# Kernel optimization log

Hardware: AMD Instinct MI355X
Metric: run time of the kernel (lower is better)

The kernel has to match this reference:

```python
import jax, jax.numpy as jnp
import numpy as np

DEPTH = 8
DIM = 512
D_INNER = 2 * DIM          # mamba expand=2
D_STATE = 16
D_CONV = 4
DT_RANK = DIM // 16        # 32
B, H, W = 2, 16, 16
EPS = 1e-5


def setup_inputs() -> dict:
    key = jax.random.key(0)
    ks = jax.random.split(key, 8)
    s = 0.02
    f32 = jnp.float32
    x = jax.random.normal(ks[0], (B, DIM, H, W), f32)
    in_proj_w = (jax.random.normal(ks[1], (DEPTH, 2 * D_INNER, DIM), f32) * s)
    conv_w = (jax.random.normal(ks[2], (DEPTH, D_INNER, D_CONV), f32) * 0.1)
    conv_b = jnp.zeros((DEPTH, D_INNER), f32)
    x_proj_w = (jax.random.normal(ks[3], (DEPTH, DT_RANK + 2 * D_STATE, D_INNER), f32) * s)
    dt_proj_w = (jax.random.normal(ks[4], (DEPTH, D_INNER, DT_RANK), f32) * s)
    dt_proj_b = (jax.random.normal(ks[5], (DEPTH, D_INNER), f32) * 0.1)
    # S4D-real init: A = -exp(A_log), A_log = log(1..d_state)
    A_log = jnp.log(jnp.broadcast_to(
        jnp.arange(1, D_STATE + 1, dtype=f32), (DEPTH, D_INNER, D_STATE)))
    D = jnp.ones((DEPTH, D_INNER), f32)
    out_proj_w = (jax.random.normal(ks[6], (DEPTH, DIM, D_INNER), f32) * s)
    norm_w = jnp.ones((DEPTH, DIM), f32)
    final_norm_w = jnp.ones((DIM,), f32)
    return {"x": x, "in_proj_w": in_proj_w, "conv_w": conv_w, "conv_b": conv_b,
            "x_proj_w": x_proj_w, "dt_proj_w": dt_proj_w, "dt_proj_b": dt_proj_b,
            "A_log": A_log, "D": D, "out_proj_w": out_proj_w,
            "norm_w": norm_w, "final_norm_w": final_norm_w}


def _rmsnorm(x, w):
    # rms_norm_ref: no mean subtraction, weight only (bias is None)
    return x * jax.lax.rsqrt(jnp.mean(x * x, axis=-1, keepdims=True) + EPS) * w


def _mixer(h, Wi, cw, cb, Wx, Wdt, bdt, A_log, Dv, Wo):
    # h: [B, L, DIM]
    xz = jnp.einsum('bld,ed->ble', h, Wi)            # [B,L,2*Di]
    xc, z = jnp.split(xz, 2, axis=-1)
    # causal depthwise conv1d (pad left d_conv-1), then SiLU
    xt = xc.transpose(0, 2, 1)                        # [B,Di,L]
    xt = jax.lax.conv_general_dilated(
        xt, cw[:, None, :], (1,), [(D_CONV - 1, 0)],
        feature_group_count=D_INNER)
    xc = jax.nn.silu((xt + cb[None, :, None]).transpose(0, 2, 1))  # [B,L,Di]
    dbl = jnp.einsum('bld,kd->blk', xc, Wx)           # [B,L,dt_rank+2N]
    dtr = dbl[..., :DT_RANK]
    Bm = dbl[..., DT_RANK:DT_RANK + D_STATE]          # [B,L,N]
    Cm = dbl[..., DT_RANK + D_STATE:]                 # [B,L,N]
    dt = jax.nn.softplus(jnp.einsum('blr,dr->bld', dtr, Wdt) + bdt)  # [B,L,Di]
    A = -jnp.exp(A_log)                               # [Di,N]
    dA = jnp.exp(dt[..., None] * A)                   # [B,L,Di,N]
    dBx = (dt * xc)[..., None] * Bm[:, :, None, :]    # [B,L,Di,N]

    def step(s, inp):
        a, bx, c = inp
        s = a * s + bx                                # [B,Di,N]
        return s, jnp.einsum('bdn,bn->bd', s, c)

    s0 = jnp.zeros((xc.shape[0], D_INNER, D_STATE), xc.dtype)
    _, ys = jax.lax.scan(step, s0, (dA.transpose(1, 0, 2, 3),
                                    dBx.transpose(1, 0, 2, 3),
                                    Cm.transpose(1, 0, 2)))
    y = ys.transpose(1, 0, 2) + Dv * xc               # [B,L,Di]
    y = y * jax.nn.silu(z)
    return jnp.einsum('bld,od->blo', y, Wo)           # [B,L,DIM]


def reference(x, in_proj_w, conv_w, conv_b, x_proj_w, dt_proj_w, dt_proj_b,
              A_log, D, out_proj_w, norm_w, final_norm_w):
    Bz, C, Hh, Ww = x.shape
    h = x.reshape(Bz, C, Hh * Ww).transpose(0, 2, 1)  # [B,L,C]
    residual = None
    for i in range(DEPTH):
        # fused add + RMSNorm (prenorm): residual <- h + residual; hn = norm(residual)
        residual = h if residual is None else h + residual
        hn = _rmsnorm(residual, norm_w[i])
        h = _mixer(hn, in_proj_w[i], conv_w[i], conv_b[i], x_proj_w[i],
                   dt_proj_w[i], dt_proj_b[i], A_log[i], D[i], out_proj_w[i])
    # Original module: with return_index=[depth-1], the returned tensor is the
    # post-loop `residual`; the final mixer output and final norm are dead code.
    out = residual.reshape(Bz, Hh, Ww, C)
    return out.transpose(0, 3, 1, 2)
```

## Files before the change

### kernel.cpp

```cpp
#include <hip/hip_runtime.h>
#include <hip/hip_bf16.h>

typedef __bf16 bf16x8 __attribute__((ext_vector_type(8)));
typedef float  f32x4  __attribute__((ext_vector_type(4)));
typedef unsigned short ushort8v __attribute__((ext_vector_type(8)));

#define DIM    512
#define DINNER 1024
#define SEQL   256
#define NLAYER 7
#define LPAD   260
#define NCH    8
#define CLEN   32

#define N4WI (NLAYER * 2048 * 512 / 4)
#define N4WX (NLAYER * 64 * 1024 / 4)
#define N4WO (NLAYER * 512 * 1024 / 4)
#define N4ALL (N4WI + N4WX + N4WO)
#define NCASTB (N4ALL / 256)

__global__ __launch_bounds__(256) void k_castin(const float* __restrict__ Wi,
                                                const float* __restrict__ Wx,
                                                const float* __restrict__ Wo,
                                                const float* __restrict__ x,
                                                __hip_bfloat16* __restrict__ wib,
                                                __hip_bfloat16* __restrict__ wxb,
                                                __hip_bfloat16* __restrict__ wob,
                                                float* __restrict__ res) {
  if (blockIdx.x >= NCASTB) {
    int idx = (blockIdx.x - NCASTB) * 256 + threadIdx.x;
    int d = idx & (DIM - 1), l = (idx >> 9) & (SEQL - 1), b = idx >> 17;
    res[idx] = x[((size_t)((b << 9) + d) << 8) + l];
    return;
  }
  int i = blockIdx.x * 256 + threadIdx.x;
  const float* src; __hip_bfloat16* dst; int j;
  if (i < N4WI)             { src = Wi; dst = wib; j = i; }
  else if (i < N4WI + N4WX) { src = Wx; dst = wxb; j = i - N4WI; }
  else                      { src = Wo; dst = wob; j = i - N4WI - N4WX; }
  float4 v = reinterpret_cast<const float4*>(src)[j];
  struct alignas(8) B4 { __hip_bfloat16 a, b, c, d; };
  B4 o{ (__hip_bfloat16)v.x, (__hip_bfloat16)v.y, (__hip_bfloat16)v.z, (__hip_bfloat16)v.w };
  reinterpret_cast<B4*>(dst)[j] = o;
}

__global__ __launch_bounds__(1024) void k_front(const float* __restrict__ res,
                                                const float* __restrict__ nwL,
                                                const __hip_bfloat16* __restrict__ wiL,
                                                const float4* __restrict__ cwL,
                                                const float* __restrict__ cbL,
                                                __hip_bfloat16* __restrict__ xcb,
                                                float* __restrict__ zT) {
  __shared__ __align__(16) char smem[75264];
  __hip_bfloat16 (*s_hn)[520] = (__hip_bfloat16(*)[520])smem;
  float (*s_xz)[132] = (float(*)[132])(smem + 49920);
  const int tid = threadIdx.x, bid = blockIdx.x;
  const int wid = tid >> 6, lane = tid & 63;
  const int r = lane & 15, g = lane >> 4;
  const int ttile = bid >> 4, sl = bid & 15;
  const int t0 = ttile * 32, m0 = t0 - 3;
#pragma unroll
  for (int k = 0; k < 3; ++k) {
    int rw = wid * 3 + k;
    int grc = min(max(m0 + rw, 0), 511);
    const float* rr = res + ((size_t)grc << 9);
    float v[8]; float ssum = 0.f;
#pragma unroll
    for (int j2 = 0; j2 < 8; ++j2) { v[j2] = rr[lane + (j2 << 6)]; ssum = fmaf(v[j2], v[j2], ssum); }
#pragma unroll
    for (int m = 1; m < 64; m <<= 1) ssum += __shfl_xor(ssum, m);
    float inv = rsqrtf(ssum * (1.0f / 512.0f) + 1e-5f);
#pragma unroll
    for (int j2 = 0; j2 < 8; ++j2)
      s_hn[rw][lane + (j2 << 6)] = (__hip_bfloat16)(v[j2] * inv * nwL[lane + (j2 << 6)]);
  }
  __syncthreads();
  for (int j = wid; j < 24; j += 16) {
    int mf = j >> 3, cf = j & 7;
    int gcol = (cf < 4) ? (sl * 64 + cf * 16 + r) : (1024 + sl * 64 + (cf - 4) * 16 + r);
    const bf16x8* pb = reinterpret_cast<const bf16x8*>(wiL + (size_t)gcol * 512) + g;
    f32x4 acc = {0.f, 0.f, 0.f, 0.f};
#pragma unroll
    for (int kc = 0; kc < 16; ++kc) {
      bf16x8 a = *reinterpret_cast<const bf16x8*>(&s_hn[mf * 16 + r][kc * 32 + g * 8]);
      acc = __builtin_amdgcn_mfma_f32_16x16x32_bf16(a, pb[kc * 4], acc, 0, 0, 0);
    }
    int cc = (cf < 4) ? (cf * 16 + r) : (64 + (cf - 4) * 16 + r);
#pragma unroll
    for (int jj = 0; jj < 4; ++jj) s_xz[mf * 16 + g * 4 + jj][cc] = acc[jj];
  }
  __syncthreads();
  const int t0s = t0 & 255;
#pragma unroll
  for (int k = 0; k < 2; ++k) {
    int e = tid + (k << 10);
    int lloc = e >> 6, c = e & 63;
    int gd = sl * 64 + c;
    int lseq = t0s + lloc;
    float4 wv = cwL[gd];
    float accv = cbL[gd];
    accv = fmaf(s_xz[lloc + 3][c], wv.w, accv);
    if (lseq >= 1) accv = fmaf(s_xz[lloc + 2][c], wv.z, accv);
    if (lseq >= 2) accv = fmaf(s_xz[lloc + 1][c], wv.y, accv);
    if (lseq >= 3) accv = fmaf(s_xz[lloc + 0][c], wv.x, accv);
    float sv = accv / (1.f + __expf(-accv));
    xcb[(size_t)(t0 + lloc) * 1024 + gd] = (__hip_bfloat16)sv;
  }
  __syncthreads();
#pragma unroll
  for (int k = 0; k < 2; ++k) {
    int e = tid + (k << 10);
    int lloc = e & 31, c = e >> 5;
    int gd = sl * 64 + c;
    zT[(size_t)gd * 512 + t0 + lloc] = s_xz[lloc + 3][64 + c];
  }
}

__global__ __launch_bounds__(1024) void k_xdt(const __hip_bfloat16* __restrict__ xcb,
                                              const __hip_bfloat16* __restrict__ wxL,
                                              float* __restrict__ dblBC,
                                              __hip_bfloat16* __restrict__ dtrb) {
  __shared__ __align__(16) float s_red[4 * 1088];
  const int tid = threadIdx.x, bid = blockIdx.x;
  const int wid = tid >> 6, lane = tid & 63;
  const int r = lane & 15, g = lane >> 4;
  const int t0 = bid * 16;
  {
    int nf = wid >> 2, ks = wid & 3;
    const bf16x8* pa = reinterpret_cast<const bf16x8*>(xcb + (size_t)(t0 + r) * 1024) + ks * 32 + g;
    const bf16x8* pb = reinterpret_cast<const bf16x8*>(wxL + (size_t)(nf * 16 + r) * 1024) + ks * 32 + g;
    f32x4 acc = {0.f, 0.f, 0.f, 0.f};
#pragma unroll
    for (int kc = 0; kc < 8; ++kc)
      acc = __builtin_amdgcn_mfma_f32_16x16x32_bf16(pa[kc * 4], pb[kc * 4], acc, 0, 0, 0);
#pragma unroll
    for (int jj = 0; jj < 4; ++jj)
      s_red[ks * 1088 + (g * 4 + jj) * 68 + nf * 16 + r] = acc[jj];
  }
  __syncthreads();
  {
    int row = tid >> 6, col = tid & 63;
    float dsum = s_red[row * 68 + col] + s_red[1088 + row * 68 + col]
               + s_red[2176 + row * 68 + col] + s_red[3264 + row * 68 + col];
    if (col >= 32) dblBC[((size_t)(t0 + row) << 5) + (col - 32)] = dsum;
    else           dtrb [((size_t)(t0 + row) << 5) + col] = (__hip_bfloat16)dsum;
  }
}

__global__ __launch_bounds__(1024) void k_scan(const float* __restrict__ dblBC,
                                               const __hip_bfloat16* __restrict__ dtrb,
                                               const float* __restrict__ WdtL,
                                               const float* __restrict__ bdtL,
                                               const __hip_bfloat16* __restrict__ xcb,
                                               const float* __restrict__ zT,
                                               const float* __restrict__ alog,
                                               const float* __restrict__ dv,
                                               __hip_bfloat16* __restrict__ y) {
  __shared__ __align__(16) char smem[127744];
  float (*s_dt)[LPAD] = (float(*)[LPAD])(smem);
  float (*s_xc)[LPAD] = (float(*)[LPAD])(smem + 8320);
  float (*s_B)[LPAD]  = (float(*)[LPAD])(smem + 16640);
  float (*s_C)[LPAD]  = (float(*)[LPAD])(smem + 33280);
  float (*s_cp)[68]   = (float(*)[68]) (smem + 49920);
  float (*s_pe)[128]  = (float(*)[128])(smem + 119552);
  float (*s_se)[128]  = (float(*)[128])(smem + 123648);
  const int tid = threadIdx.x, bid = blockIdx.x;
  const int cg = tid >> 7;
  const int tt = tid & 127;
  const int n = tt & 15, dl = tt >> 4;
  const int b = bid >> 7;
  const int d0 = (bid & 127) << 3;
  const int d = d0 + dl;
  const int bL = b * SEQL;

#pragma unroll
  for (int k = 0; k < 2; ++k) {
    int fidx = tid + (k << 10);
    int l = fidx >> 3, q = fidx & 7;
    float4 v = *reinterpret_cast<const float4*>(dblBC + ((size_t)(bL + l) << 5) + (q << 2));
    float* dst = (q < 4) ? &s_B[(q & 3) << 2][l] : &s_C[(q & 3) << 2][l];
    dst[0] = v.x; dst[LPAD] = v.y; dst[2 * LPAD] = v.z; dst[3 * LPAD] = v.w;
  }
  if (tid < 256) {
    bf16x8 u = *reinterpret_cast<const bf16x8*>(xcb + (size_t)(bL + tid) * 1024 + d0);
#pragma unroll
    for (int e = 0; e < 8; ++e) s_xc[e][tid] = (float)u[e];
  }
  {
    int tk = tid >> 2;
    int cp = (tid & 3) << 1;
    const ushort8v* drp = reinterpret_cast<const ushort8v*>(
        reinterpret_cast<const unsigned short*>(dtrb) + ((size_t)(bL + tk) << 5));
    float xv[32];
#pragma unroll
    for (int q = 0; q < 4; ++q) {
      ushort8v u = drp[q];
#pragma unroll
      for (int e = 0; e < 8; ++e)
        xv[q * 8 + e] = __uint_as_float(((unsigned int)u[e]) << 16);
    }
#pragma unroll
    for (int kk = 0; kk < 2; ++kk) {
      int ch = cp + kk;
      const float4* wr = reinterpret_cast<const float4*>(WdtL + ((size_t)(d0 + ch) << 5));
      float acc = bdtL[d0 + ch];
#pragma unroll
      for (int q = 0; q < 8; ++q) {
        float4 w = wr[q];
        acc = fmaf(xv[q * 4 + 0], w.x, acc);
        acc = fmaf(xv[q * 4 + 1], w.y, acc);
        acc = fmaf(xv[q * 4 + 2], w.z, acc);
        acc = fmaf(xv[q * 4 + 3], w.w, acc);
      }
      s_dt[ch][tk] = (acc > 20.f) ? acc : log1pf(__expf(acc));
    }
  }
  __syncthreads();

  const float An = -__expf(alog[(size_t)d * 16 + n]);
  const int lb = cg << 5;

  float s = 0.f, P = 1.f;
#pragma unroll 2
  for (int l4 = 0; l4 < CLEN; l4 += 4) {
    const int l = lb + l4;
    float4 dt4 = *reinterpret_cast<const float4*>(&s_dt[dl][l]);
    float4 xc4 = *reinterpret_cast<const float4*>(&s_xc[dl][l]);
    float4 B4  = *reinterpret_cast<const float4*>(&s_B[n][l]);
    float dA;
    dA = __expf(dt4.x * An); P *= dA; s = fmaf(dA, s, dt4.x * xc4.x * B4.x);
    dA = __expf(dt4.y * An); P *= dA; s = fmaf(dA, s, dt4.y * xc4.y * B4.y);
    dA = __expf(dt4.z * An); P *= dA; s = fmaf(dA, s, dt4.z * xc4.z * B4.z);
    dA = __expf(dt4.w * An); P *= dA; s = fmaf(dA, s, dt4.w * xc4.w * B4.w);
  }
  s_pe[cg][tt] = P;
  s_se[cg][tt] = s;
  __syncthreads();

  float ss = 0.f;
  for (int c = 0; c < cg; ++c) ss = fmaf(s_pe[c][tt], ss, s_se[c][tt]);

  float s2 = ss;
#pragma unroll 2
  for (int l4 = 0; l4 < CLEN; l4 += 4) {
    const int l = lb + l4;
    float4 dt4 = *reinterpret_cast<const float4*>(&s_dt[dl][l]);
    float4 xc4 = *reinterpret_cast<const float4*>(&s_xc[dl][l]);
    float4 B4  = *reinterpret_cast<const float4*>(&s_B[n][l]);
    float4 C4  = *reinterpret_cast<const float4*>(&s_C[n][l]);
    float dA, c;
    dA = __expf(dt4.x * An); s2 = fmaf(dA, s2, dt4.x * xc4.x * B4.x); c = s2 * C4.x;
    c += __shfl_xor(c, 1); if (!(n & 1)) s_cp[l + 0][(dl << 3) | (n >> 1)] = c;
    dA = __expf(dt4.y * An); s2 = fmaf(dA, s2, dt4.y * xc4.y * B4.y); c = s2 * C4.y;
    c += __shfl_xor(c, 1); if (!(n & 1)) s_cp[l + 1][(dl << 3) | (n >> 1)] = c;
    dA = __expf(dt4.z * An); s2 = fmaf(dA, s2, dt4.z * xc4.z * B4.z); c = s2 * C4.z;
    c += __shfl_xor(c, 1); if (!(n & 1)) s_cp[l + 2][(dl << 3) | (n >> 1)] = c;
    dA = __expf(dt4.w * An); s2 = fmaf(dA, s2, dt4.w * xc4.w * B4.w); c = s2 * C4.w;
    c += __shfl_xor(c, 1); if (!(n & 1)) s_cp[l + 3][(dl << 3) | (n >> 1)] = c;
  }
  __syncthreads();

#pragma unroll
  for (int k = 0; k < 2; ++k) {
    int idx = tid + (k << 10);
    int l = idx >> 3, dd = idx & 7;
    const float* cr = &s_cp[l][dd << 3];
    float4 a0 = *reinterpret_cast<const float4*>(cr);
    float4 a1 = *reinterpret_cast<const float4*>(cr + 4);
    float sum = ((a0.x + a0.y) + (a0.z + a0.w)) + ((a1.x + a1.y) + (a1.z + a1.w));
    float xcv = s_xc[dd][l];
    float zv = zT[(size_t)(d0 + dd) * 512 + bL + l];
    float yv = (sum + dv[d0 + dd] * xcv) * (zv / (1.f + __expf(-zv)));
    y[((size_t)(bL + l) << 10) + d0 + dd] = (__hip_bfloat16)yv;
  }
}

template <bool FINAL>
__global__ __launch_bounds__(1024) void k_outproj(const __hip_bfloat16* __restrict__ y,
                                                  const __hip_bfloat16* __restrict__ woL,
                                                  float* __restrict__ res,
                                                  float* __restrict__ out) {
  __shared__ __align__(16) float s_red[16 * 1088 + 32 * 33];
  float (*s_tr)[33] = (float(*)[33])(s_red + 16 * 1088);
  const int tid = threadIdx.x, bid = blockIdx.x;
  const int wid = tid >> 6, lane = tid & 63;
  const int r = lane & 15, g = lane >> 4;
  int tile = bid >> 2, q = bid & 3;
  int row0 = (tile >> 3) * 64 + ((q >> 1) << 5);
  int col0 = (tile & 7) * 64 + ((q & 1) << 5);
  {
    const bf16x8* pa0 = reinterpret_cast<const bf16x8*>(y + (size_t)(row0 + r) * 1024) + g + wid * 8;
    const bf16x8* pa1 = reinterpret_cast<const bf16x8*>(y + (size_t)(row0 + 16 + r) * 1024) + g + wid * 8;
    const bf16x8* pb0 = reinterpret_cast<const bf16x8*>(woL + (size_t)(col0 + r) * 1024) + g + wid * 8;
    const bf16x8* pb1 = reinterpret_cast<const bf16x8*>(woL + (size_t)(col0 + 16 + r) * 1024) + g + wid * 8;
    f32x4 zz = {0.f, 0.f, 0.f, 0.f};
    f32x4 acc[4] = {zz, zz, zz, zz};
#pragma unroll
    for (int kc = 0; kc < 2; ++kc) {
      bf16x8 a0 = pa0[kc * 4], a1 = pa1[kc * 4];
      bf16x8 b0 = pb0[kc * 4], b1 = pb1[kc * 4];
      acc[0] = __builtin_amdgcn_mfma_f32_16x16x32_bf16(a0, b0, acc[0], 0, 0, 0);
      acc[1] = __builtin_amdgcn_mfma_f32_16x16x32_bf16(a0, b1, acc[1], 0, 0, 0);
      acc[2] = __builtin_amdgcn_mfma_f32_16x16x32_bf16(a1, b0, acc[2], 0, 0, 0);
      acc[3] = __builtin_amdgcn_mfma_f32_16x16x32_bf16(a1, b1, acc[3], 0, 0, 0);
    }
    float* sr = s_red + wid * 1088;
#pragma unroll
    for (int e = 0; e < 4; ++e)
#pragma unroll
      for (int jj = 0; jj < 4; ++jj)
        sr[(((e >> 1) << 4) + (g << 2) + jj) * 34 + ((e & 1) << 4) + r] = acc[e][jj];
  }
  __syncthreads();
  {
    int rrow = tid >> 5, rcol = tid & 31;
    float sum = 0.f;
#pragma unroll
    for (int w = 0; w < 16; ++w) sum += s_red[w * 1088 + rrow * 34 + rcol];
    if (!FINAL) {
      res[(size_t)(row0 + rrow) * 512 + col0 + rcol] += sum;
    } else {
      s_tr[rcol][rrow] = res[(size_t)(row0 + rrow) * 512 + col0 + rcol] + sum;
    }
  }
  if (FINAL) {
    __syncthreads();
    int tl = tid & 31, tc = tid >> 5;
    int b = row0 >> 8, l0 = row0 & 255;
    out[(((size_t)((b << 9) + col0 + tc)) << 8) | (l0 + tl)] = s_tr[tc][tl];
  }
}

extern "C" void kernel_launch(void* const* d_in, const int* in_sizes, int n_in,
                              void* d_out, int out_size, void* d_ws, size_t ws_size,
                              hipStream_t stream) {
  (void)in_sizes; (void)n_in; (void)out_size; (void)ws_size;
  const float* x    = (const float*)d_in[0];
  const float* Wi   = (const float*)d_in[1];
  const float* cw   = (const float*)d_in[2];
  const float* cb   = (const float*)d_in[3];
  const float* Wx   = (const float*)d_in[4];
  const float* Wdt  = (const float*)d_in[5];
  const float* bdt  = (const float*)d_in[6];
  const float* Alog = (const float*)d_in[7];
  const float* Dv   = (const float*)d_in[8];
  const float* Wo   = (const float*)d_in[9];
  const float* nw   = (const float*)d_in[10];

  char* ws = (char*)d_ws;
  float*          res   = (float*)(ws + 0);
  __hip_bfloat16* xcb   = (__hip_bfloat16*)(ws + 1048576);
  float*          zT    = (float*)(ws + 4194304);
  __hip_bfloat16* dtrb  = (__hip_bfloat16*)(ws + 6291456);
  float*          dblBC = (float*)(ws + 8388608);
  __hip_bfloat16* y     = (__hip_bfloat16*)(ws + 8454144);
  __hip_bfloat16* wib   = (__hip_bfloat16*)(ws + 10485760);
  __hip_bfloat16* wxb   = (__hip_bfloat16*)(ws + 25165824);
  __hip_bfloat16* wob   = (__hip_bfloat16*)(ws + 26083328);

  k_castin<<<NCASTB + 1024, 256, 0, stream>>>(Wi, Wx, Wo, x, wib, wxb, wob, res);

  for (int L = 0; L < NLAYER; ++L) {
    k_front<<<256, 1024, 0, stream>>>(res, nw + L * DIM,
                                      wib + (size_t)L * 2048 * 512,
                                      (const float4*)cw + (size_t)L * DINNER,
                                      cb + L * DINNER, xcb, zT);
    k_xdt<<<32, 1024, 0, stream>>>(xcb, wxb + (size_t)L * 64 * 1024, dblBC, dtrb);
    k_scan<<<256, 1024, 0, stream>>>(dblBC, dtrb,
                                     Wdt + (size_t)L * DINNER * 32, bdt + L * DINNER,
                                     xcb, zT,
                                     Alog + (size_t)L * DINNER * 16, Dv + L * DINNER, y);
    if (L < NLAYER - 1)
      k_outproj<false><<<256, 1024, 0, stream>>>(y, wob + (size_t)L * 512 * 1024, res, nullptr);
    else
      k_outproj<true><<<256, 1024, 0, stream>>>(y, wob + (size_t)L * 512 * 1024, res, (float*)d_out);
  }
}
```

Measured before the change: 352.5 us.

## Fuse x_proj GEMM into front kernel with split-K atomic accumulation

Removes the separate x_proj kernel. Each front block now multiplies its 32x64 slice of the conv output, held in shared memory, against the matching slice of the x_proj weights and atomically adds the partial sums into an fp32 buffer. The buffer is zeroed in the cast kernel and again in each out-projection launch. The scan kernel now reads dt_rank, B and C all in fp32 from that buffer, which saves one kernel launch per layer and a global round trip of the conv output, at the cost of 16-way atomic contention per element and nondeterministic summation order.

```diff
diff --git a/kernel.cpp b/kernel.cpp
--- a/kernel.cpp
+++ b/kernel.cpp
@@ -3,7 +3,6 @@
 
 typedef __bf16 bf16x8 __attribute__((ext_vector_type(8)));
 typedef float  f32x4  __attribute__((ext_vector_type(4)));
-typedef unsigned short ushort8v __attribute__((ext_vector_type(8)));
 
 #define DIM    512
 #define DINNER 1024
@@ -26,7 +25,13 @@
                                                 __hip_bfloat16* __restrict__ wib,
                                                 __hip_bfloat16* __restrict__ wxb,
                                                 __hip_bfloat16* __restrict__ wob,
-                                                float* __restrict__ res) {
+                                                float* __restrict__ res,
+                                                float* __restrict__ dblraw) {
+  if (blockIdx.x >= NCASTB + 1024) {
+    int i = (blockIdx.x - NCASTB - 1024) * 256 + threadIdx.x;
+    reinterpret_cast<float4*>(dblraw)[i] = float4{0.f, 0.f, 0.f, 0.f};
+    return;
+  }
   if (blockIdx.x >= NCASTB) {
     int idx = (blockIdx.x - NCASTB) * 256 + threadIdx.x;
     int d = idx & (DIM - 1), l = (idx >> 9) & (SEQL - 1), b = idx >> 17;
@@ -47,13 +52,16 @@
 __global__ __launch_bounds__(1024) void k_front(const float* __restrict__ res,
                                                 const float* __restrict__ nwL,
                                                 const __hip_bfloat16* __restrict__ wiL,
+                                                const __hip_bfloat16* __restrict__ wxL,
                                                 const float4* __restrict__ cwL,
                                                 const float* __restrict__ cbL,
                                                 __hip_bfloat16* __restrict__ xcb,
-                                                float* __restrict__ zT) {
-  __shared__ __align__(16) char smem[75264];
+                                                float* __restrict__ zT,
+                                                float* __restrict__ dblraw) {
+  __shared__ __align__(16) char smem[79872];
   __hip_bfloat16 (*s_hn)[520] = (__hip_bfloat16(*)[520])smem;
   float (*s_xz)[132] = (float(*)[132])(smem + 49920);
+  __hip_bfloat16 (*s_xcb)[72] = (__hip_bfloat16(*)[72])(smem + 75264);
   const int tid = threadIdx.x, bid = blockIdx.x;
   const int wid = tid >> 6, lane = tid & 63;
   const int r = lane & 15, g = lane >> 4;
@@ -104,51 +112,36 @@
     if (lseq >= 2) accv = fmaf(s_xz[lloc + 1][c], wv.y, accv);
     if (lseq >= 3) accv = fmaf(s_xz[lloc + 0][c], wv.x, accv);
     float sv = accv / (1.f + __expf(-accv));
-    xcb[(size_t)(t0 + lloc) * 1024 + gd] = (__hip_bfloat16)sv;
-  }
-  __syncthreads();
-#pragma unroll
-  for (int k = 0; k < 2; ++k) {
-    int e = tid + (k << 10);
-    int lloc = e & 31, c = e >> 5;
-    int gd = sl * 64 + c;
-    zT[(size_t)gd * 512 + t0 + lloc] = s_xz[lloc + 3][64 + c];
-  }
-}
-
-__global__ __launch_bounds__(1024) void k_xdt(const __hip_bfloat16* __restrict__ xcb,
-                                              const __hip_bfloat16* __restrict__ wxL,
-                                              float* __restrict__ dblBC,
-                                              __hip_bfloat16* __restrict__ dtrb) {
-  __shared__ __align__(16) float s_red[4 * 1088];
-  const int tid = threadIdx.x, bid = blockIdx.x;
-  const int wid = tid >> 6, lane = tid & 63;
-  const int r = lane & 15, g = lane >> 4;
-  const int t0 = bid * 16;
-  {
-    int nf = wid >> 2, ks = wid & 3;
-    const bf16x8* pa = reinterpret_cast<const bf16x8*>(xcb + (size_t)(t0 + r) * 1024) + ks * 32 + g;
-    const bf16x8* pb = reinterpret_cast<const bf16x8*>(wxL + (size_t)(nf * 16 + r) * 1024) + ks * 32 + g;
+    __hip_bfloat16 hb = (__hip_bfloat16)sv;
+    xcb[(size_t)(t0 + lloc) * 1024 + gd] = hb;
+    s_xcb[lloc][c] = hb;
+  }
+  __syncthreads();
+  if (wid < 8) {
+    int mf = wid & 1, nf = wid >> 1;
     f32x4 acc = {0.f, 0.f, 0.f, 0.f};
 #pragma unroll
-    for (int kc = 0; kc < 8; ++kc)
-      acc = __builtin_amdgcn_mfma_f32_16x16x32_bf16(pa[kc * 4], pb[kc * 4], acc, 0, 0, 0);
+    for (int kc = 0; kc < 2; ++kc) {
+      bf16x8 a = *reinterpret_cast<const bf16x8*>(&s_xcb[mf * 16 + r][kc * 32 + g * 8]);
+      bf16x8 bb = *reinterpret_cast<const bf16x8*>(
+          wxL + (size_t)(nf * 16 + r) * 1024 + sl * 64 + kc * 32 + g * 8);
+      acc = __builtin_amdgcn_mfma_f32_16x16x32_bf16(a, bb, acc, 0, 0, 0);
+    }
 #pragma unroll
     for (int jj = 0; jj < 4; ++jj)
-      s_red[ks * 1088 + (g * 4 + jj) * 68 + nf * 16 + r] = acc[jj];
-  }
-  __syncthreads();
-  {
-    int row = tid >> 6, col = tid & 63;
-    float dsum = s_red[row * 68 + col] + s_red[1088 + row * 68 + col]
-               + s_red[2176 + row * 68 + col] + s_red[3264 + row * 68 + col];
-    if (col >= 32) dblBC[((size_t)(t0 + row) << 5) + (col - 32)] = dsum;
-    else           dtrb [((size_t)(t0 + row) << 5) + col] = (__hip_bfloat16)dsum;
-  }
-}
-
-__global__ __launch_bounds__(1024) void k_scan(const float* __restrict__ dblBC,
-                                               const __hip_bfloat16* __restrict__ dtrb,
+      atomicAdd(&dblraw[(size_t)(t0 + mf * 16 + g * 4 + jj) * 64 + nf * 16 + r], acc[jj]);
+  } else {
+#pragma unroll
+    for (int k = 0; k < 4; ++k) {
+      int e = (tid - 512) + (k << 9);
+      int lloc = e & 31, c = e >> 5;
+      int gd = sl * 64 + c;
+      zT[(size_t)gd * 512 + t0 + lloc] = s_xz[lloc + 3][64 + c];
+    }
+  }
+}
+
+__global__ __launch_bounds__(1024) void k_scan(const float* __restrict__ dblraw,
                                                const float* __restrict__ WdtL,
                                                const float* __restrict__ bdtL,
                                                const __hip_bfloat16* __restrict__ xcb,
@@ -177,7 +170,7 @@
   for (int k = 0; k < 2; ++k) {
     int fidx = tid + (k << 10);
     int l = fidx >> 3, q = fidx & 7;
-    float4 v = *reinterpret_cast<const float4*>(dblBC + ((size_t)(bL + l) << 5) + (q << 2));
+    float4 v = *reinterpret_cast<const float4*>(dblraw + ((size_t)(bL + l) << 6) + 32 + (q << 2));
     float* dst = (q < 4) ? &s_B[(q & 3) << 2][l] : &s_C[(q & 3) << 2][l];
     dst[0] = v.x; dst[LPAD] = v.y; dst[2 * LPAD] = v.z; dst[3 * LPAD] = v.w;
   }
@@ -189,15 +182,13 @@
   {
     int tk = tid >> 2;
     int cp = (tid & 3) << 1;
-    const ushort8v* drp = reinterpret_cast<const ushort8v*>(
-        reinterpret_cast<const unsigned short*>(dtrb) + ((size_t)(bL + tk) << 5));
+    const float* drow = dblraw + ((size_t)(bL + tk) << 6);
     float xv[32];
 #pragma unroll
-    for (int q = 0; q < 4; ++q) {
-      ushort8v u = drp[q];
-#pragma unroll
-      for (int e = 0; e < 8; ++e)
-        xv[q * 8 + e] = __uint_as_float(((unsigned int)u[e]) << 16);
+    for (int q = 0; q < 8; ++q) {
+      float4 x4 = *reinterpret_cast<const float4*>(drow + (q << 2));
+      xv[q * 4 + 0] = x4.x; xv[q * 4 + 1] = x4.y;
+      xv[q * 4 + 2] = x4.z; xv[q * 4 + 3] = x4.w;
     }
 #pragma unroll
     for (int kk = 0; kk < 2; ++kk) {
@@ -279,7 +270,8 @@
 __global__ __launch_bounds__(1024) void k_outproj(const __hip_bfloat16* __restrict__ y,
                                                   const __hip_bfloat16* __restrict__ woL,
                                                   float* __restrict__ res,
-                                                  float* __restrict__ out) {
+                                                  float* __restrict__ out,
+                                                  float* __restrict__ dblraw) {
   __shared__ __align__(16) float s_red[16 * 1088 + 32 * 33];
   float (*s_tr)[33] = (float(*)[33])(s_red + 16 * 1088);
   const int tid = threadIdx.x, bid = blockIdx.x;
@@ -288,6 +280,8 @@
   int tile = bid >> 2, q = bid & 3;
   int row0 = (tile >> 3) * 64 + ((q >> 1) << 5);
   int col0 = (tile & 7) * 64 + ((q & 1) << 5);
+  if (!FINAL && tid < 32)
+    reinterpret_cast<float4*>(dblraw)[bid * 32 + tid] = float4{0.f, 0.f, 0.f, 0.f};
   {
     const bf16x8* pa0 = reinterpret_cast<const bf16x8*>(y + (size_t)(row0 + r) * 1024) + g + wid * 8;
     const bf16x8* pa1 = reinterpret_cast<const bf16x8*>(y + (size_t)(row0 + 16 + r) * 1024) + g + wid * 8;
@@ -348,31 +342,33 @@
   const float* nw   = (const float*)d_in[10];
 
   char* ws = (char*)d_ws;
-  float*          res   = (float*)(ws + 0);
-  __hip_bfloat16* xcb   = (__hip_bfloat16*)(ws + 1048576);
-  float*          zT    = (float*)(ws + 4194304);
-  __hip_bfloat16* dtrb  = (__hip_bfloat16*)(ws + 6291456);
-  float*          dblBC = (float*)(ws + 8388608);
-  __hip_bfloat16* y     = (__hip_bfloat16*)(ws + 8454144);
-  __hip_bfloat16* wib   = (__hip_bfloat16*)(ws + 10485760);
-  __hip_bfloat16* wxb   = (__hip_bfloat16*)(ws + 25165824);
-  __hip_bfloat16* wob   = (__hip_bfloat16*)(ws + 26083328);
-
-  k_castin<<<NCASTB + 1024, 256, 0, stream>>>(Wi, Wx, Wo, x, wib, wxb, wob, res);
+  float*          res    = (float*)(ws + 0);
+  __hip_bfloat16* xcb    = (__hip_bfloat16*)(ws + 1048576);
+  float*          zT     = (float*)(ws + 4194304);
+  float*          dblraw = (float*)(ws + 6291456);
+  __hip_bfloat16* y      = (__hip_bfloat16*)(ws + 8454144);
+  __hip_bfloat16* wib    = (__hip_bfloat16*)(ws + 10485760);
+  __hip_bfloat16* wxb    = (__hip_bfloat16*)(ws + 25165824);
+  __hip_bfloat16* wob    = (__hip_bfloat16*)(ws + 26083328);
+
+  k_castin<<<NCASTB + 1024 + 32, 256, 0, stream>>>(Wi, Wx, Wo, x, wib, wxb, wob,
+                                                   res, dblraw);
 
   for (int L = 0; L < NLAYER; ++L) {
     k_front<<<256, 1024, 0, stream>>>(res, nw + L * DIM,
                                       wib + (size_t)L * 2048 * 512,
+                                      wxb + (size_t)L * 64 * 1024,
                                       (const float4*)cw + (size_t)L * DINNER,
-                                      cb + L * DINNER, xcb, zT);
-    k_xdt<<<32, 1024, 0, stream>>>(xcb, wxb + (size_t)L * 64 * 1024, dblBC, dtrb);
-    k_scan<<<256, 1024, 0, stream>>>(dblBC, dtrb,
+                                      cb + L * DINNER, xcb, zT, dblraw);
+    k_scan<<<256, 1024, 0, stream>>>(dblraw,
                                      Wdt + (size_t)L * DINNER * 32, bdt + L * DINNER,
                                      xcb, zT,
                                      Alog + (size_t)L * DINNER * 16, Dv + L * DINNER, y);
     if (L < NLAYER - 1)
-      k_outproj<false><<<256, 1024, 0, stream>>>(y, wob + (size_t)L * 512 * 1024, res, nullptr);
+      k_outproj<false><<<256, 1024, 0, stream>>>(y, wob + (size_t)L * 512 * 1024, res,
+                                                 nullptr, dblraw);
     else
-      k_outproj<true><<<256, 1024, 0, stream>>>(y, wob + (size_t)L * 512 * 1024, res, (float*)d_out);
-  }
-}
+      k_outproj<true><<<256, 1024, 0, stream>>>(y, wob + (size_t)L * 512 * 1024, res,
+                                                (float*)d_out, dblraw);
+  }
+}
```

New measurement: 306.5 us. 13.0% less time.
